# Kernel optimization log

Measured on AMD Instinct MI355X. Metric: run time of the kernel, lower is better.

The kernel has to match this reference:

```python
import jax, jax.numpy as jnp
import numpy as np

B, T, NIN, H1, H2, E, A = 256, 128, 1024, 512, 512, 256, 16
EPS = 1e-5


def setup_inputs() -> dict:
    key = jax.random.key(0)
    ks = jax.random.split(key, 24)
    def lin(k, fan_in, fan_out):
        # weights stored [in, out]; y = x @ W + b (equivalent to torch Linear)
        s = 1.0 / np.sqrt(fan_in)
        kw, kb = jax.random.split(k)
        return (jax.random.uniform(kw, (fan_in, fan_out), jnp.float32, -s, s),
                jax.random.uniform(kb, (fan_out,), jnp.float32, -s, s))
    W1, b1 = lin(ks[0], NIN, H1)
    W2, b2 = lin(ks[1], H1, H2)
    W3, b3 = lin(ks[2], H2, E)
    Wih, bih = lin(ks[3], E, 3 * E)   # GRUCell input weights, gate order [r, z, n]
    Whh, bhh = lin(ks[4], E, 3 * E)   # GRUCell hidden weights
    Whe, bhe = lin(ks[5], E + A, E)   # hidden_encoder
    Wae, bae = lin(ks[6], A, A)       # action_encoder
    return {
        'obs': jax.random.normal(ks[7], (B, T, NIN), jnp.float32),
        'actions': jax.random.normal(ks[8], (B, T, A), jnp.float32),
        'W1': W1, 'b1': b1, 'g1': jnp.ones((H1,), jnp.float32), 'be1': jnp.zeros((H1,), jnp.float32),
        'W2': W2, 'b2': b2, 'g2': jnp.ones((H2,), jnp.float32), 'be2': jnp.zeros((H2,), jnp.float32),
        'W3': W3, 'b3': b3,
        'Wih': Wih, 'bih': bih, 'Whh': Whh, 'bhh': bhh,
        'Whe': Whe, 'bhe': bhe, 'Wae': Wae, 'bae': bae,
    }


def reference(obs, actions, W1, b1, g1, be1, W2, b2, g2, be2, W3, b3,
              Wih, bih, Whh, bhh, Whe, bhe, Wae, bae):
    def bn(x, g, b):  # BatchNorm1d, training mode (batch stats, biased var)
        mu = jnp.mean(x, axis=0)
        var = jnp.mean((x - mu) ** 2, axis=0)
        return g * (x - mu) / jnp.sqrt(var + EPS) + b

    def mlp(x):
        x = jax.nn.elu(bn(x @ W1 + b1, g1, be1))
        x = jax.nn.elu(bn(x @ W2 + b2, g2, be2))
        return x @ W3 + b3

    def gru(x, h):
        gi = x @ Wih + bih
        gh = h @ Whh + bhh
        ir, iz, inn = jnp.split(gi, 3, axis=1)
        hr, hz, hn = jnp.split(gh, 3, axis=1)
        r = jax.nn.sigmoid(ir + hr)
        z = jax.nn.sigmoid(iz + hz)
        n = jnp.tanh(inn + r * hn)
        return (1.0 - z) * n + z * h

    obs_t = jnp.swapaxes(obs, 0, 1)       # [T, B, NIN]
    act_t = jnp.swapaxes(actions, 0, 1)   # [T, B, A]
    h0 = jnp.zeros((obs.shape[0], E), jnp.float32)
    a0 = jnp.zeros((obs.shape[0], A), jnp.float32)

    def step(carry, xs):
        h, a_prev = carry
        o, a = xs
        h = jnp.concatenate([h, a_prev], axis=1) @ Whe + bhe
        a_prev = a @ Wae + bae
        h = gru(mlp(o), h)
        return (h, a_prev), None

    (h, _), _ = jax.lax.scan(step, (h0, a0), (obs_t, act_t))
    return h
```

## Files before the change

### kernel.cpp

```cpp
#include <hip/hip_runtime.h>
#include <math.h>
#include <stdint.h>

#define B_   256
#define T_   128
#define NIN_ 1024
#define H1_  512
#define E_   256
#define A_   16
#define MT_  (B_ * T_)

typedef unsigned short ushort_t;
typedef unsigned long long ull_t;
typedef __attribute__((ext_vector_type(8))) short   short8;
typedef __attribute__((ext_vector_type(8))) __bf16  bf16x8;
typedef __attribute__((ext_vector_type(4))) float   f32x4;

union frag8 { short8 s; bf16x8 b; };

__device__ __forceinline__ ushort_t f2bf(float f) {
  union { float f; unsigned u; } v; v.f = f;
  unsigned r = (v.u + 0x7FFFu + ((v.u >> 16) & 1u)) >> 16;
  return (ushort_t)r;
}

static constexpr size_t OFF_C0    = 0;
static constexpr size_t OFF_OBSB  = 0;
static constexpr size_t OFF_Y     = 134217728;
static constexpr size_t OFF_XGP   = 167772160;
static constexpr size_t OFF_XB    = 201326592;
static constexpr size_t OFF_INN   = 201326592;
static constexpr size_t OFF_AE    = 234881024;
static constexpr size_t OFF_W1T   = 236978176;
static constexpr size_t OFF_W2T   = 238026752;
static constexpr size_t OFF_W3T   = 238551040;
static constexpr size_t OFF_WC    = 239075328;
static constexpr size_t OFF_WCT   = 240123904;
static constexpr size_t OFF_BSUM  = 241172480;
static constexpr size_t OFF_FLAGS = 241176576;
static constexpr size_t OFF_HG    = 241238016;


__global__ __launch_bounds__(256) void cast_obs_k(const float* __restrict__ obs,
                                                  ushort_t* __restrict__ out) {
  int row_in = blockIdx.x;
  int b = row_in / T_, t = row_in - b * T_;
  const float4* s4 = (const float4*)(obs + (size_t)row_in * NIN_);
  float4 v = s4[threadIdx.x];
  ushort_t* d = out + (size_t)(t * B_ + b) * NIN_ + threadIdx.x * 4;
  d[0] = f2bf(v.x); d[1] = f2bf(v.y); d[2] = f2bf(v.z); d[3] = f2bf(v.w);
}

__global__ __launch_bounds__(256) void transpose_cast_k(const float* __restrict__ in,
                                                        ushort_t* __restrict__ out,
                                                        int R, int C, int ldo) {
  __shared__ float tile[32][33];
  int c0 = blockIdx.x * 32, r0 = blockIdx.y * 32;
  int tx = threadIdx.x & 31, ty = threadIdx.x >> 5;
  for (int i = 0; i < 4; i++) {
    int r = r0 + ty * 4 + i;
    if (r < R && (c0 + tx) < C) tile[ty * 4 + i][tx] = in[(size_t)r * C + c0 + tx];
  }
  __syncthreads();
  for (int i = 0; i < 4; i++) {
    int c = c0 + ty * 4 + i, r = r0 + tx;
    if (c < C && r < R) out[(size_t)c * ldo + r] = f2bf(tile[tx][ty * 4 + i]);
  }
}

__global__ __launch_bounds__(256) void wct_a_k(const float* __restrict__ Whe,
                                               ushort_t* __restrict__ Wct) {
  int c = blockIdx.x, k = threadIdx.x;
  Wct[(size_t)c * 256 + k] = f2bf(Whe[(size_t)k * 256 + c]);
}

__global__ __launch_bounds__(256) void wct_b_k(const float* __restrict__ Whe,
                                               const float* __restrict__ Whh,
                                               ushort_t* __restrict__ Wct) {
  int c = blockIdx.x;
  int k = threadIdx.x;
  float acc = 0.f;
  for (int j = 0; j < 256; j++)
    acc += Whe[(size_t)k * 256 + j] * Whh[(size_t)j * 768 + c];
  Wct[(size_t)(256 + c) * 256 + k] = f2bf(acc);
}

__global__ void bsum_k(const float* __restrict__ bih, const float* __restrict__ bhh,
                       float* __restrict__ bs) {
  int i = blockIdx.x * 256 + threadIdx.x;
  if (i < 768) bs[i] = bih[i] + bhh[i];
}

__global__ void init_flags_k(unsigned* f) {
  if (threadIdx.x < 16) f[threadIdx.x * 32] = 0u;
}

__global__ __launch_bounds__(256) void ae_k(const float* __restrict__ actions,
                                            const float* __restrict__ Wae,
                                            const float* __restrict__ bae,
                                            float* __restrict__ AE) {
  int idx = blockIdx.x * 256 + threadIdx.x;
  int m = idx >> 4, k2 = idx & 15;
  int t = m >> 8, b = m & 255;
  const float* arow = actions + ((size_t)b * T_ + t) * A_;
  float acc = bae[k2];
  for (int k = 0; k < 16; k++) acc += arow[k] * Wae[k * 16 + k2];
  AE[(size_t)m * 16 + k2] = acc;
}

__global__ __launch_bounds__(256) void penc_k(const float* __restrict__ AE,
                                              const float* __restrict__ Whe,
                                              const float* __restrict__ bhe,
                                              float* __restrict__ C0,
                                              ushort_t* __restrict__ XGP) {
  int m = blockIdx.x;
  int j = threadIdx.x;
  __shared__ float a[16];
  if (threadIdx.x < 16)
    a[threadIdx.x] = (m >= B_) ? AE[(size_t)(m - B_) * 16 + threadIdx.x] : 0.f;
  __syncthreads();
  float acc = bhe[j];
  if (m >= B_) {
    for (int k = 0; k < 16; k++) acc += a[k] * Whe[(size_t)(256 + k) * 256 + j];
  }
  C0[(size_t)m * 1024 + j] = acc;
  XGP[(size_t)m * 512 + 256 + j] = f2bf(acc);
}

__global__ __launch_bounds__(256) void bn_elu_k(const float* __restrict__ Y,
                                                const float* __restrict__ g,
                                                const float* __restrict__ be,
                                                ushort_t* __restrict__ Xb) {
  int t = blockIdx.x, f = blockIdx.y * 256 + threadIdx.x;
  const float* base = Y + (size_t)t * B_ * H1_;
  float s = 0.f, ss = 0.f;
  for (int b = 0; b < B_; b++) {
    float v = base[(size_t)b * H1_ + f];
    s += v; ss += v * v;
  }
  float mu  = s * (1.f / B_);
  float var = ss * (1.f / B_) - mu * mu;
  float inv = 1.f / sqrtf(var + 1e-5f);
  float sc = g[f] * inv, sh = be[f] - mu * sc;
  ushort_t* ob = Xb + (size_t)t * B_ * H1_;
  for (int b = 0; b < B_; b++) {
    float v = base[(size_t)b * H1_ + f] * sc + sh;
    float e = v > 0.f ? v : (expf(v) - 1.f);
    ob[(size_t)b * H1_ + f] = f2bf(e);
  }
}

__global__ __launch_bounds__(256) void gemm_bt_k(const ushort_t* __restrict__ A, int lda,
                                                 const ushort_t* __restrict__ Bt, int ldb,
                                                 float* __restrict__ C,
                                                 ushort_t* __restrict__ Cb, int ldc,
                                                 const float* __restrict__ bias,
                                                 int K, int accum) {
  __shared__ __align__(16) ushort_t As[128][40];
  __shared__ __align__(16) ushort_t Bs[128][40];
  int tid = threadIdx.x;
  int wave = tid >> 6, lane = tid & 63;
  int q = lane >> 4, l15 = lane & 15;
  int wr = wave >> 1, wc = wave & 1;
  int m0 = blockIdx.x * 128, n0 = blockIdx.y * 128;
  f32x4 acc[4][4] = {};
  int r = tid >> 1, sh = (tid & 1) * 16;
  const ushort_t* aSrc = A + (size_t)(m0 + r) * lda + sh;
  const ushort_t* bSrc = Bt + (size_t)(n0 + r) * ldb + sh;
  for (int k0 = 0; k0 < K; k0 += 32) {
    *(short8*)&As[r][sh]     = *(const short8*)(aSrc + k0);
    *(short8*)&As[r][sh + 8] = *(const short8*)(aSrc + k0 + 8);
    *(short8*)&Bs[r][sh]     = *(const short8*)(bSrc + k0);
    *(short8*)&Bs[r][sh + 8] = *(const short8*)(bSrc + k0 + 8);
    __syncthreads();
    frag8 af[4], bf[4];
#pragma unroll
    for (int i = 0; i < 4; i++) {
      af[i].s = *(const short8*)&As[wr * 64 + i * 16 + l15][q * 8];
      bf[i].s = *(const short8*)&Bs[wc * 64 + i * 16 + l15][q * 8];
    }
#pragma unroll
    for (int at = 0; at < 4; at++)
#pragma unroll
      for (int bt = 0; bt < 4; bt++)
        acc[at][bt] = __builtin_amdgcn_mfma_f32_16x16x32_bf16(af[at].b, bf[bt].b, acc[at][bt], 0, 0, 0);
    __syncthreads();
  }
#pragma unroll
  for (int at = 0; at < 4; at++)
#pragma unroll
    for (int bt = 0; bt < 4; bt++) {
      int mb = m0 + wr * 64 + at * 16 + q * 4;
      int n  = n0 + wc * 64 + bt * 16 + l15;
      float bv = bias ? bias[n] : 0.f;
#pragma unroll
      for (int i = 0; i < 4; i++) {
        size_t idx = (size_t)(mb + i) * ldc + n;
        float v = acc[at][bt][i] + bv;
        if (Cb) {
          Cb[idx] = f2bf(v);
        } else {
          if (accum) v += C[idx];
          C[idx] = v;
        }
      }
    }
}

__global__ __launch_bounds__(1024) void gru_cols_k(
    const ushort_t* __restrict__ Wct,
    const float* __restrict__ C0,
    const float* __restrict__ INN,
    ull_t* __restrict__ hG,
    unsigned* __restrict__ flags,
    float* __restrict__ outF) {
  __shared__ __align__(16) ushort_t Wb[256][264];
  __shared__ __align__(16) ushort_t h_lds[16][264];
  __shared__ float G[4][16][66];

  const int tid = threadIdx.x;
  const int w = tid >> 6, lane = tid & 63;
  const int q = lane >> 4, l15 = lane & 15;
  const int rg = blockIdx.x & 15, cg = blockIdx.x >> 4;
  const int r0 = rg * 16;
  const int g = w >> 2, j = w & 3;

  unsigned* flag = flags + rg * 32;

  for (int d = tid; d < 16 * 264 / 2; d += 1024) ((unsigned*)h_lds)[d] = 0u;
  for (int i = tid; i < 256 * 32; i += 1024) {
    int rr = i >> 5, ss = i & 31;
    int srow = (rr >> 6) * 256 + cg * 64 + (rr & 63);
    *(short8*)&Wb[rr][ss * 8] = *(const short8*)(Wct + (size_t)srow * 256 + ss * 8);
  }
  __syncthreads();

  const int crow = w;
  const int ccol = lane;
  const int hg = cg * 64 + ccol;

  for (int t = 0; t < T_; t++) {
    const float* c0t  = C0  + ((size_t)t * B_ + r0) * 1024;
    const float* innt = INN + ((size_t)t * B_ + r0) * 256;
    float c0he = c0t[(size_t)crow * 1024 + hg];
    float c0r  = c0t[(size_t)crow * 1024 + 256 + hg];
    float c0z  = c0t[(size_t)crow * 1024 + 512 + hg];
    float c0hn = c0t[(size_t)crow * 1024 + 768 + hg];
    float c0in = innt[(size_t)crow * 256 + hg];

    if (t > 0) {
      if (tid == 0) {
        unsigned target = 4u * (unsigned)t;
        while (__hip_atomic_load(flag, __ATOMIC_ACQUIRE, __HIP_MEMORY_SCOPE_AGENT) < target)
          __builtin_amdgcn_s_sleep(1);
      }
      __syncthreads();
      if (tid < 768) {
        int s = tid >> 8;
        int cgs = s + (s >= cg ? 1 : 0);
        int rem = tid & 255;
        int row = rem >> 4, cp = rem & 15;
        ull_t v = __hip_atomic_load(&hG[(size_t)(t & 1) * 256 * 64 + (size_t)(r0 + row) * 64 + cgs * 16 + cp],
                                    __ATOMIC_RELAXED, __HIP_MEMORY_SCOPE_AGENT);
        *(ull_t*)&h_lds[row][cgs * 64 + cp * 4] = v;
      }
      __syncthreads();
    }

    f32x4 acc = {};
#pragma unroll
    for (int kc = 0; kc < 8; kc++) {
      frag8 a, b;
      a.s = *(const short8*)&h_lds[l15][kc * 32 + q * 8];
      b.s = *(const short8*)&Wb[g * 64 + j * 16 + l15][kc * 32 + q * 8];
      acc = __builtin_amdgcn_mfma_f32_16x16x32_bf16(a.b, b.b, acc, 0, 0, 0);
    }
#pragma unroll
    for (int i = 0; i < 4; i++) G[g][q * 4 + i][j * 16 + l15] = acc[i];
    __syncthreads();

    float henc = G[0][crow][ccol] + c0he;
    float rp   = G[1][crow][ccol] + c0r;
    float zp   = G[2][crow][ccol] + c0z;
    float hn   = G[3][crow][ccol] + c0hn;
    float rgate = 1.f / (1.f + expf(-rp));
    float zgate = 1.f / (1.f + expf(-zp));
    float ng = tanhf(c0in + rgate * hn);
    float hv = (1.f - zgate) * ng + zgate * henc;

    if (t < T_ - 1) {
      h_lds[crow][cg * 64 + ccol] = f2bf(hv);
      __syncthreads();
      if (tid < 256) {
        int row2 = tid >> 4, cp = tid & 15;
        ull_t v = *(const ull_t*)&h_lds[row2][cg * 64 + cp * 4];
        __hip_atomic_store(&hG[(size_t)((t + 1) & 1) * 256 * 64 + (size_t)(r0 + row2) * 64 + cg * 16 + cp],
                           v, __ATOMIC_RELAXED, __HIP_MEMORY_SCOPE_AGENT);
      }
      __syncthreads();
      if (tid == 0)
        __hip_atomic_fetch_add(flag, 1u, __ATOMIC_RELEASE, __HIP_MEMORY_SCOPE_AGENT);
    } else {
      outF[(size_t)(r0 + crow) * 256 + hg] = hv;
    }
  }
}

extern "C" void kernel_launch(void* const* d_in, const int* in_sizes, int n_in,
                              void* d_out, int out_size, void* d_ws, size_t ws_size,
                              hipStream_t stream) {
  const float* obs     = (const float*)d_in[0];
  const float* actions = (const float*)d_in[1];
  const float* W1  = (const float*)d_in[2];
  const float* b1  = (const float*)d_in[3];
  const float* g1  = (const float*)d_in[4];
  const float* be1 = (const float*)d_in[5];
  const float* W2  = (const float*)d_in[6];
  const float* b2  = (const float*)d_in[7];
  const float* g2  = (const float*)d_in[8];
  const float* be2 = (const float*)d_in[9];
  const float* W3  = (const float*)d_in[10];
  const float* b3  = (const float*)d_in[11];
  const float* Wih = (const float*)d_in[12];
  const float* bih = (const float*)d_in[13];
  const float* Whh = (const float*)d_in[14];
  const float* bhh = (const float*)d_in[15];
  const float* Whe = (const float*)d_in[16];
  const float* bhe = (const float*)d_in[17];
  const float* Wae = (const float*)d_in[18];
  const float* bae = (const float*)d_in[19];

  char* ws = (char*)d_ws;
  float*    C0    = (float*)(ws + OFF_C0);
  ushort_t* obsb  = (ushort_t*)(ws + OFF_OBSB);
  float*    Y     = (float*)(ws + OFF_Y);
  ushort_t* XGP   = (ushort_t*)(ws + OFF_XGP);
  ushort_t* Xb    = (ushort_t*)(ws + OFF_XB);
  float*    INN   = (float*)(ws + OFF_INN);
  float*    AE    = (float*)(ws + OFF_AE);
  ushort_t* W1t   = (ushort_t*)(ws + OFF_W1T);
  ushort_t* W2t   = (ushort_t*)(ws + OFF_W2T);
  ushort_t* W3t   = (ushort_t*)(ws + OFF_W3T);
  ushort_t* WC    = (ushort_t*)(ws + OFF_WC);
  ushort_t* Wct   = (ushort_t*)(ws + OFF_WCT);
  float*    bsum  = (float*)(ws + OFF_BSUM);
  unsigned* flags = (unsigned*)(ws + OFF_FLAGS);
  ull_t*    hG    = (ull_t*)(ws + OFF_HG);
  float*    outF  = (float*)d_out;

  cast_obs_k<<<MT_, 256, 0, stream>>>(obs, obsb);
  transpose_cast_k<<<dim3(16, 32), 256, 0, stream>>>(W1, W1t, 1024, 512, 1024);
  transpose_cast_k<<<dim3(16, 16), 256, 0, stream>>>(W2, W2t, 512, 512, 512);
  transpose_cast_k<<<dim3(8, 16),  256, 0, stream>>>(W3, W3t, 512, 256, 512);
  transpose_cast_k<<<dim3(24, 8),  256, 0, stream>>>(Wih, WC, 256, 768, 512);
  transpose_cast_k<<<dim3(24, 8),  256, 0, stream>>>(Whh, WC + 256, 256, 768, 512);
  wct_a_k<<<256, 256, 0, stream>>>(Whe, Wct);
  wct_b_k<<<768, 256, 0, stream>>>(Whe, Whh, Wct);
  bsum_k<<<3, 256, 0, stream>>>(bih, bhh, bsum);
  init_flags_k<<<1, 64, 0, stream>>>(flags);
  ae_k<<<MT_ * 16 / 256, 256, 0, stream>>>(actions, Wae, bae, AE);

  gemm_bt_k<<<dim3(256, 4), 256, 0, stream>>>(obsb, 1024, W1t, 1024, Y, nullptr, 512, b1, 1024, 0);
  bn_elu_k<<<dim3(T_, 2), 256, 0, stream>>>(Y, g1, be1, Xb);
  gemm_bt_k<<<dim3(256, 4), 256, 0, stream>>>(Xb, 512, W2t, 512, Y, nullptr, 512, b2, 512, 0);
  bn_elu_k<<<dim3(T_, 2), 256, 0, stream>>>(Y, g2, be2, Xb);
  gemm_bt_k<<<dim3(256, 2), 256, 0, stream>>>(Xb, 512, W3t, 512, nullptr, XGP, 512, b3, 512, 0);

  penc_k<<<MT_, 256, 0, stream>>>(AE, Whe, bhe, C0, XGP);
  gemm_bt_k<<<dim3(256, 4), 256, 0, stream>>>(XGP, 512, WC, 512, C0 + 256, nullptr, 1024, bsum, 512, 0);
  gemm_bt_k<<<dim3(256, 2), 256, 0, stream>>>(XGP + 256, 512, WC + 512 * 512 + 256, 512, C0 + 768, nullptr, 1024, bhh + 512, 256, 0);
  gemm_bt_k<<<dim3(256, 2), 256, 0, stream>>>(XGP, 512, WC + 512 * 512, 512, INN, nullptr, 256, bih + 512, 256, 0);

  gru_cols_k<<<64, 1024, 0, stream>>>(Wct, C0, INN, hG, flags, outF);
}
```

Measured before the change: 1.115 ms.

## Use direct global-to-LDS loads in GEMM and overlap own-slice GRU MFMA with wait

The GEMM tile loads now go straight from global memory into LDS through global_load_lds, with no padding, instead of passing through registers. In the recurrent GRU kernel, each block runs the MFMA over the k-chunks covering its own hidden slice before it waits on the cross-block flag. Only the remaining chunks are computed after the exchanged hidden state arrives. This is meant to cut register staging and shorten the serial critical path per timestep, but removing the LDS padding may bring back bank conflicts on the fragment reads.

```diff
diff --git a/kernel.cpp b/kernel.cpp
--- a/kernel.cpp
+++ b/kernel.cpp
@@ -22,6 +22,11 @@
   union { float f; unsigned u; } v; v.f = f;
   unsigned r = (v.u + 0x7FFFu + ((v.u >> 16) & 1u)) >> 16;
   return (ushort_t)r;
+}
+
+__device__ __forceinline__ void gl_lds16(const ushort_t* g, ushort_t* l) {
+  __builtin_amdgcn_global_load_lds((const __attribute__((address_space(1))) void*)g,
+                                   (__attribute__((address_space(3))) void*)l, 16, 0, 0);
 }
 
 static constexpr size_t OFF_C0    = 0;
@@ -156,28 +161,29 @@
                                                  ushort_t* __restrict__ Cb, int ldc,
                                                  const float* __restrict__ bias,
                                                  int K, int accum) {
-  __shared__ __align__(16) ushort_t As[128][40];
-  __shared__ __align__(16) ushort_t Bs[128][40];
+  __shared__ __align__(16) ushort_t As[128 * 32];
+  __shared__ __align__(16) ushort_t Bs[128 * 32];
   int tid = threadIdx.x;
   int wave = tid >> 6, lane = tid & 63;
   int q = lane >> 4, l15 = lane & 15;
   int wr = wave >> 1, wc = wave & 1;
   int m0 = blockIdx.x * 128, n0 = blockIdx.y * 128;
   f32x4 acc[4][4] = {};
-  int r = tid >> 1, sh = (tid & 1) * 16;
-  const ushort_t* aSrc = A + (size_t)(m0 + r) * lda + sh;
-  const ushort_t* bSrc = Bt + (size_t)(n0 + r) * ldb + sh;
+  const int rbase = wave * 32;
+  const int srow = lane >> 2, seg = lane & 3;
+  const ushort_t* aS = A + (size_t)(m0 + rbase + srow) * lda + seg * 8;
+  const ushort_t* bS = Bt + (size_t)(n0 + rbase + srow) * ldb + seg * 8;
   for (int k0 = 0; k0 < K; k0 += 32) {
-    *(short8*)&As[r][sh]     = *(const short8*)(aSrc + k0);
-    *(short8*)&As[r][sh + 8] = *(const short8*)(aSrc + k0 + 8);
-    *(short8*)&Bs[r][sh]     = *(const short8*)(bSrc + k0);
-    *(short8*)&Bs[r][sh + 8] = *(const short8*)(bSrc + k0 + 8);
+    gl_lds16(aS + k0,                      &As[rbase * 32]);
+    gl_lds16(aS + (size_t)16 * lda + k0,   &As[(rbase + 16) * 32]);
+    gl_lds16(bS + k0,                      &Bs[rbase * 32]);
+    gl_lds16(bS + (size_t)16 * ldb + k0,   &Bs[(rbase + 16) * 32]);
     __syncthreads();
     frag8 af[4], bf[4];
 #pragma unroll
     for (int i = 0; i < 4; i++) {
-      af[i].s = *(const short8*)&As[wr * 64 + i * 16 + l15][q * 8];
-      bf[i].s = *(const short8*)&Bs[wc * 64 + i * 16 + l15][q * 8];
+      af[i].s = *(const short8*)&As[(wr * 64 + i * 16 + l15) * 32 + q * 8];
+      bf[i].s = *(const short8*)&Bs[(wc * 64 + i * 16 + l15) * 32 + q * 8];
     }
 #pragma unroll
     for (int at = 0; at < 4; at++)
@@ -238,6 +244,7 @@
   const int crow = w;
   const int ccol = lane;
   const int hg = cg * 64 + ccol;
+  const int kcown = cg * 2;
 
   for (int t = 0; t < T_; t++) {
     const float* c0t  = C0  + ((size_t)t * B_ + r0) * 1024;
@@ -247,6 +254,16 @@
     float c0z  = c0t[(size_t)crow * 1024 + 512 + hg];
     float c0hn = c0t[(size_t)crow * 1024 + 768 + hg];
     float c0in = innt[(size_t)crow * 256 + hg];
+
+    f32x4 acc = {};
+#pragma unroll
+    for (int e = 0; e < 2; e++) {
+      int kc = kcown + e;
+      frag8 a, b;
+      a.s = *(const short8*)&h_lds[l15][kc * 32 + q * 8];
+      b.s = *(const short8*)&Wb[g * 64 + j * 16 + l15][kc * 32 + q * 8];
+      acc = __builtin_amdgcn_mfma_f32_16x16x32_bf16(a.b, b.b, acc, 0, 0, 0);
+    }
 
     if (t > 0) {
       if (tid == 0) {
@@ -267,9 +284,9 @@
       __syncthreads();
     }
 
-    f32x4 acc = {};
 #pragma unroll
     for (int kc = 0; kc < 8; kc++) {
+      if (kc == kcown || kc == kcown + 1) continue;
       frag8 a, b;
       a.s = *(const short8*)&h_lds[l15][kc * 32 + q * 8];
       b.s = *(const short8*)&Wb[g * 64 + j * 16 + l15][kc * 32 + q * 8];
```

New measurement: 1.091 ms. 2.2% less time.
